# Performance work log

Measured on AMD Instinct MI355X. Metric: run time of the kernel, lower is better.

## Reference

```python
import jax, jax.numpy as jnp
import numpy as np

SM_SCALE = 0.07216878364870322  # 1/sqrt(192)
PAGE_SIZE = 64


def setup_inputs() -> dict:
    key = jax.random.key(0)
    ks = jax.random.split(key, 6)
    B, Hq, Hkv = 32, 16, 1
    DN, DR, DV = 128, 64, 128
    NUM_PAGES, MAX_PAGES = 2048, 64
    return {
        "q": jax.random.normal(ks[0], (B, Hq, DN + DR), dtype=jnp.float32),
        "k_nope_buffer": jax.random.normal(ks[1], (NUM_PAGES, PAGE_SIZE, Hkv, DN), dtype=jnp.float32),
        "k_rope_buffer": jax.random.normal(ks[2], (NUM_PAGES, PAGE_SIZE, Hkv, DR), dtype=jnp.float32),
        "v_buffer": jax.random.normal(ks[3], (NUM_PAGES, PAGE_SIZE, Hkv, DV), dtype=jnp.float32),
        "seq_lens": jax.random.randint(ks[4], (B,), 1, MAX_PAGES * PAGE_SIZE + 1, dtype=jnp.int32),
        "block_table": jax.random.randint(ks[5], (B, MAX_PAGES), 0, NUM_PAGES, dtype=jnp.int32),
    }


def reference(q, k_nope_buffer, k_rope_buffer, v_buffer, seq_lens, block_table):
    B, Hq, _ = q.shape
    Hkv = k_nope_buffer.shape[2]
    dn = k_nope_buffer.shape[-1]
    dv = v_buffer.shape[-1]
    max_kv = block_table.shape[1] * PAGE_SIZE

    q_nope = q[:, :, :dn]            # (B, Hq, dn)
    q_rope = q[:, :, dn:]            # (B, Hq, dr)

    # Gather pages per batch: (B, max_pages, page, Hkv, d) -> (B, max_kv, Hkv, d)
    kn = k_nope_buffer[block_table].reshape(B, max_kv, Hkv, dn)
    kr = k_rope_buffer[block_table].reshape(B, max_kv, Hkv, -1)
    v = v_buffer[block_table].reshape(B, max_kv, Hkv, dv)

    rep = Hq // Hkv  # GQA repeat_interleave == repeat along head axis
    if rep != 1:
        kn = jnp.repeat(kn, rep, axis=2)
        kr = jnp.repeat(kr, rep, axis=2)
        v = jnp.repeat(v, rep, axis=2)

    scores = (jnp.einsum('bhd,bkhd->bhk', q_nope, kn)
              + jnp.einsum('bhd,bkhd->bhk', q_rope, kr)).astype(jnp.float32) * SM_SCALE
    # Mask out key positions beyond each sequence length (replaces per-batch slicing)
    valid = jnp.arange(max_kv)[None, None, :] < seq_lens[:, None, None]
    scores = jnp.where(valid, scores, -jnp.inf)
    probs = jax.nn.softmax(scores, axis=-1).astype(v.dtype)  # (B, Hq, max_kv)
    out = jnp.einsum('bhk,bkhd->bhd', probs, v)              # (B, Hq, dv)
    return out
```

## Files before the change

### kernel.cpp

```cpp
#include <hip/hip_runtime.h>
#include <math.h>

#define NB 32
#define HQ 16
#define DN 128
#define DR 64
#define DQT 192
#define DV 128
#define PAGE 64
#define MAXP 64
#define NSPLIT 16
#define SPLIT_PAGES 4
#define SPLIT_T (SPLIT_PAGES * PAGE)
#define SM_SCALE 0.07216878364870322f

__global__ __launch_bounds__(256, 2)
void attn_partial_kernel(const float* __restrict__ q,
                         const float* __restrict__ kn,
                         const float* __restrict__ kr,
                         const float* __restrict__ v,
                         const int* __restrict__ seq_lens,
                         const int* __restrict__ block_table,
                         float* __restrict__ o_part,
                         float* __restrict__ ml_part)
{
    const int split = blockIdx.x;
    const int b = blockIdx.y;
    const int seq = seq_lens[b];
    const int t0 = split * SPLIT_T;
    if (t0 >= seq) return;

    const int tid = (int)threadIdx.x;
    const int wave = tid >> 6;
    const int lane = tid & 63;

    __shared__ float q_s[HQ * DQT];
    __shared__ float p_s[SPLIT_T][HQ];
    __shared__ float redmax_s[SPLIT_PAGES][HQ];
    __shared__ float redsum_s[SPLIT_PAGES][HQ];
    __shared__ float acc_s[DV][HQ + 1];
    __shared__ int bt_s[SPLIT_PAGES];

    {
        const float4* qb = (const float4*)(q + (size_t)b * HQ * DQT);
        float4* qs4 = (float4*)q_s;
        #pragma unroll
        for (int i = 0; i < 3; i++) qs4[tid + 256 * i] = qb[tid + 256 * i];
    }
    if (tid < SPLIT_PAGES)
        bt_s[tid] = block_table[b * MAXP + split * SPLIT_PAGES + tid];
    __syncthreads();

    float s[HQ];
    #pragma unroll
    for (int h = 0; h < HQ; h++) s[h] = 0.f;

    const int pbase = t0 + wave * PAGE;
    const bool wave_valid = pbase < seq;
    const bool valid = (pbase + lane) < seq;

    if (wave_valid) {
        const int pid = bt_s[wave];
        const float4* knp = (const float4*)(kn + ((size_t)pid * PAGE + lane) * DN);
        #pragma unroll 8
        for (int c = 0; c < DN / 4; c++) {
            float4 k4 = knp[c];
            #pragma unroll
            for (int h = 0; h < HQ; h++) {
                float4 q4 = ((const float4*)(q_s + h * DQT))[c];
                s[h] += q4.x * k4.x + q4.y * k4.y + q4.z * k4.z + q4.w * k4.w;
            }
        }
        const float4* krp = (const float4*)(kr + ((size_t)pid * PAGE + lane) * DR);
        #pragma unroll 8
        for (int c = 0; c < DR / 4; c++) {
            float4 k4 = krp[c];
            #pragma unroll
            for (int h = 0; h < HQ; h++) {
                float4 q4 = ((const float4*)(q_s + h * DQT))[DN / 4 + c];
                s[h] += q4.x * k4.x + q4.y * k4.y + q4.z * k4.z + q4.w * k4.w;
            }
        }
    }
    #pragma unroll
    for (int h = 0; h < HQ; h++) s[h] = valid ? s[h] * SM_SCALE : -INFINITY;

    #pragma unroll
    for (int h = 0; h < HQ; h++) {
        float m = s[h];
        #pragma unroll
        for (int off = 32; off > 0; off >>= 1) m = fmaxf(m, __shfl_xor(m, off));
        if (lane == 0) redmax_s[wave][h] = m;
    }
    __syncthreads();

    #pragma unroll
    for (int h = 0; h < HQ; h++) {
        float m = fmaxf(fmaxf(redmax_s[0][h], redmax_s[1][h]),
                        fmaxf(redmax_s[2][h], redmax_s[3][h]));
        s[h] = __expf(s[h] - m);
    }
    {
        const int t = wave * PAGE + lane;
        float4* prow = (float4*)(&p_s[t][0]);
        #pragma unroll
        for (int j = 0; j < 4; j++) {
            float4 pv;
            pv.x = s[4 * j + 0]; pv.y = s[4 * j + 1];
            pv.z = s[4 * j + 2]; pv.w = s[4 * j + 3];
            prow[j] = pv;
        }
    }
    #pragma unroll
    for (int h = 0; h < HQ; h++) {
        float l = s[h];
        #pragma unroll
        for (int off = 32; off > 0; off >>= 1) l += __shfl_xor(l, off);
        if (lane == 0) redsum_s[wave][h] = l;
    }
    __syncthreads();

    if (tid < HQ) {
        const int h = tid;
        float m = fmaxf(fmaxf(redmax_s[0][h], redmax_s[1][h]),
                        fmaxf(redmax_s[2][h], redmax_s[3][h]));
        float l = redsum_s[0][h] + redsum_s[1][h] + redsum_s[2][h] + redsum_s[3][h];
        float* ml = ml_part + ((size_t)(b * NSPLIT + split) * HQ + h) * 2;
        ml[0] = m;
        ml[1] = l;
    }

    const int g = tid >> 7;
    const int d = tid & 127;
    float acc[HQ];
    #pragma unroll
    for (int h = 0; h < HQ; h++) acc[h] = 0.f;

    #pragma unroll
    for (int w = 0; w < SPLIT_PAGES; w++) {
        const int base = w * PAGE;
        if (t0 + base >= seq) break;
        const int pid = bt_s[w];
        int rem = seq - t0 - base;
        const int lim = rem < PAGE ? rem : PAGE;
        const float* vp = v + (size_t)pid * PAGE * DV + d;
        #pragma unroll 4
        for (int l2 = g; l2 < lim; l2 += 2) {
            float vv = vp[(size_t)l2 * DV];
            const float4* prow = (const float4*)(&p_s[base + l2][0]);
            #pragma unroll
            for (int j = 0; j < 4; j++) {
                float4 p4 = prow[j];
                acc[4 * j + 0] += p4.x * vv;
                acc[4 * j + 1] += p4.y * vv;
                acc[4 * j + 2] += p4.z * vv;
                acc[4 * j + 3] += p4.w * vv;
            }
        }
    }

    if (g == 1) {
        #pragma unroll
        for (int h = 0; h < HQ; h++) acc_s[d][h] = acc[h];
    }
    __syncthreads();
    if (g == 0) {
        float* op = o_part + ((size_t)(b * NSPLIT + split) * HQ) * DV + d;
        #pragma unroll
        for (int h = 0; h < HQ; h++)
            op[h * DV] = acc[h] + acc_s[d][h];
    }
}

__global__ __launch_bounds__(128)
void attn_combine_kernel(const float* __restrict__ o_part,
                         const float* __restrict__ ml_part,
                         const int* __restrict__ seq_lens,
                         float* __restrict__ out)
{
    const int h = blockIdx.x;
    const int b = blockIdx.y;
    const int d = (int)threadIdx.x;
    const int seq = seq_lens[b];
    int ns = (seq + SPLIT_T - 1) / SPLIT_T;
    if (ns > NSPLIT) ns = NSPLIT;

    float M = -INFINITY, den = 0.f, acc = 0.f;
    for (int s2 = 0; s2 < ns; s2++) {
        const float* ml = ml_part + ((size_t)(b * NSPLIT + s2) * HQ + h) * 2;
        float m = ml[0], l = ml[1];
        float o = o_part[((size_t)(b * NSPLIT + s2) * HQ + h) * DV + d];
        float nM = fmaxf(M, m);
        float eo = __expf(M - nM);
        float en = __expf(m - nM);
        acc = acc * eo + o * en;
        den = den * eo + l * en;
        M = nM;
    }
    out[((size_t)b * HQ + h) * DV + d] = acc / den;
}

extern "C" void kernel_launch(void* const* d_in, const int* in_sizes, int n_in,
                              void* d_out, int out_size, void* d_ws, size_t ws_size,
                              hipStream_t stream)
{
    const float* q  = (const float*)d_in[0];
    const float* kn = (const float*)d_in[1];
    const float* kr = (const float*)d_in[2];
    const float* v  = (const float*)d_in[3];
    const int* seq_lens    = (const int*)d_in[4];
    const int* block_table = (const int*)d_in[5];

    float* o_part  = (float*)d_ws;
    float* ml_part = o_part + (size_t)NB * NSPLIT * HQ * DV;

    attn_partial_kernel<<<dim3(NSPLIT, NB), 256, 0, stream>>>(
        q, kn, kr, v, seq_lens, block_table, o_part, ml_part);
    attn_combine_kernel<<<dim3(HQ, NB), 128, 0, stream>>>(
        o_part, ml_part, seq_lens, (float*)d_out);
}
```

Before: 205.9 us.

## Split attention into per-wave page work items with transposed Q in global memory

```diff
diff --git a/kernel.cpp b/kernel.cpp
--- a/kernel.cpp
+++ b/kernel.cpp
@@ -9,13 +9,26 @@
 #define DV 128
 #define PAGE 64
 #define MAXP 64
-#define NSPLIT 16
-#define SPLIT_PAGES 4
-#define SPLIT_T (SPLIT_PAGES * PAGE)
 #define SM_SCALE 0.07216878364870322f
 
+#define WAVE_LDS_FENCE() asm volatile("s_waitcnt lgkmcnt(0)" ::: "memory")
+
+__global__ __launch_bounds__(256)
+void q_transpose_kernel(const float* __restrict__ q, float* __restrict__ qT)
+{
+    int idx = blockIdx.x * 256 + threadIdx.x;
+    if (idx >= NB * 48 * HQ) return;
+    int h = idx & 15;
+    int t = idx >> 4;
+    int c4 = t % 48;
+    int b = t / 48;
+    const float4* q4 = (const float4*)q;
+    ((float4*)qT)[idx] = q4[((size_t)b * HQ + h) * 48 + c4];
+}
+
+template<int PP>
 __global__ __launch_bounds__(256, 2)
-void attn_partial_kernel(const float* __restrict__ q,
+void attn_partial_kernel(const float* __restrict__ qT,
                          const float* __restrict__ kn,
                          const float* __restrict__ kr,
                          const float* __restrict__ v,
@@ -24,50 +37,53 @@
                          float* __restrict__ o_part,
                          float* __restrict__ ml_part)
 {
-    const int split = blockIdx.x;
-    const int b = blockIdx.y;
-    const int seq = seq_lens[b];
-    const int t0 = split * SPLIT_T;
-    if (t0 >= seq) return;
-
+    constexpr int NS = MAXP / PP;
     const int tid = (int)threadIdx.x;
     const int wave = tid >> 6;
     const int lane = tid & 63;
 
-    __shared__ float q_s[HQ * DQT];
-    __shared__ float p_s[SPLIT_T][HQ];
-    __shared__ float redmax_s[SPLIT_PAGES][HQ];
-    __shared__ float redsum_s[SPLIT_PAGES][HQ];
-    __shared__ float acc_s[DV][HQ + 1];
-    __shared__ int bt_s[SPLIT_PAGES];
-
-    {
-        const float4* qb = (const float4*)(q + (size_t)b * HQ * DQT);
-        float4* qs4 = (float4*)q_s;
-        #pragma unroll
-        for (int i = 0; i < 3; i++) qs4[tid + 256 * i] = qb[tid + 256 * i];
-    }
-    if (tid < SPLIT_PAGES)
-        bt_s[tid] = block_table[b * MAXP + split * SPLIT_PAGES + tid];
-    __syncthreads();
-
-    float s[HQ];
+    const int item = blockIdx.x * 4 + wave;
+    const int b = item / NS;
+    const int chunk = item % NS;
+    const int page0 = chunk * PP;
+
+    const int seq = seq_lens[b];
+    if (page0 * PAGE >= seq) return;
+
+    __shared__ float p_s[4][PAGE][HQ];
+
+    const float4* qTb = (const float4*)qT + (size_t)b * 48 * HQ;
+
+    float m_run[HQ], l_run[HQ];
+    float4 accv[HQ];
     #pragma unroll
-    for (int h = 0; h < HQ; h++) s[h] = 0.f;
-
-    const int pbase = t0 + wave * PAGE;
-    const bool wave_valid = pbase < seq;
-    const bool valid = (pbase + lane) < seq;
-
-    if (wave_valid) {
-        const int pid = bt_s[wave];
+    for (int h = 0; h < HQ; h++) {
+        m_run[h] = -INFINITY; l_run[h] = 0.f;
+        accv[h] = make_float4(0.f, 0.f, 0.f, 0.f);
+    }
+
+    const int tg = lane >> 5;
+    const int dq = (lane & 31) * 4;
+
+    #pragma unroll
+    for (int pg = 0; pg < PP; pg++) {
+        const int page = page0 + pg;
+        if (page * PAGE >= seq) break;
+        const int pid = block_table[b * MAXP + page];
+        const bool valid = page * PAGE + lane < seq;
+
+        float s[HQ];
+        #pragma unroll
+        for (int h = 0; h < HQ; h++) s[h] = 0.f;
+
         const float4* knp = (const float4*)(kn + ((size_t)pid * PAGE + lane) * DN);
         #pragma unroll 8
         for (int c = 0; c < DN / 4; c++) {
             float4 k4 = knp[c];
+            const float4* qc = qTb + c * HQ;
             #pragma unroll
             for (int h = 0; h < HQ; h++) {
-                float4 q4 = ((const float4*)(q_s + h * DQT))[c];
+                float4 q4 = qc[h];
                 s[h] += q4.x * k4.x + q4.y * k4.y + q4.z * k4.z + q4.w * k4.w;
             }
         }
@@ -75,126 +91,117 @@
         #pragma unroll 8
         for (int c = 0; c < DR / 4; c++) {
             float4 k4 = krp[c];
+            const float4* qc = qTb + (DN / 4 + c) * HQ;
             #pragma unroll
             for (int h = 0; h < HQ; h++) {
-                float4 q4 = ((const float4*)(q_s + h * DQT))[DN / 4 + c];
+                float4 q4 = qc[h];
                 s[h] += q4.x * k4.x + q4.y * k4.y + q4.z * k4.z + q4.w * k4.w;
             }
         }
-    }
-    #pragma unroll
-    for (int h = 0; h < HQ; h++) s[h] = valid ? s[h] * SM_SCALE : -INFINITY;
+        #pragma unroll
+        for (int h = 0; h < HQ; h++) s[h] = valid ? s[h] * SM_SCALE : -INFINITY;
+
+        float alpha[HQ];
+        #pragma unroll
+        for (int h = 0; h < HQ; h++) {
+            float m = s[h];
+            #pragma unroll
+            for (int off = 32; off > 0; off >>= 1) m = fmaxf(m, __shfl_xor(m, off));
+            float m_new = fmaxf(m_run[h], m);
+            alpha[h] = __expf(m_run[h] - m_new);
+            m_run[h] = m_new;
+            s[h] = __expf(s[h] - m_new);
+            float l = s[h];
+            #pragma unroll
+            for (int off = 32; off > 0; off >>= 1) l += __shfl_xor(l, off);
+            l_run[h] = l_run[h] * alpha[h] + l;
+        }
+
+        WAVE_LDS_FENCE();
+        {
+            float4* prow = (float4*)(&p_s[wave][lane][0]);
+            #pragma unroll
+            for (int j = 0; j < 4; j++)
+                prow[j] = make_float4(s[4*j+0], s[4*j+1], s[4*j+2], s[4*j+3]);
+        }
+        WAVE_LDS_FENCE();
+
+        #pragma unroll
+        for (int h = 0; h < HQ; h++) {
+            accv[h].x *= alpha[h]; accv[h].y *= alpha[h];
+            accv[h].z *= alpha[h]; accv[h].w *= alpha[h];
+        }
+        const float* vp = v + (size_t)pid * PAGE * DV + dq;
+        #pragma unroll 4
+        for (int t = tg; t < PAGE; t += 2) {
+            float4 v4 = *(const float4*)(vp + (size_t)t * DV);
+            const float4* prow = (const float4*)(&p_s[wave][t][0]);
+            #pragma unroll
+            for (int j = 0; j < 4; j++) {
+                float4 p4 = prow[j];
+                accv[4*j+0].x += p4.x * v4.x; accv[4*j+0].y += p4.x * v4.y;
+                accv[4*j+0].z += p4.x * v4.z; accv[4*j+0].w += p4.x * v4.w;
+                accv[4*j+1].x += p4.y * v4.x; accv[4*j+1].y += p4.y * v4.y;
+                accv[4*j+1].z += p4.y * v4.z; accv[4*j+1].w += p4.y * v4.w;
+                accv[4*j+2].x += p4.z * v4.x; accv[4*j+2].y += p4.z * v4.y;
+                accv[4*j+2].z += p4.z * v4.z; accv[4*j+2].w += p4.z * v4.w;
+                accv[4*j+3].x += p4.w * v4.x; accv[4*j+3].y += p4.w * v4.y;
+                accv[4*j+3].z += p4.w * v4.z; accv[4*j+3].w += p4.w * v4.w;
+            }
+        }
+    }
 
     #pragma unroll
     for (int h = 0; h < HQ; h++) {
-        float m = s[h];
-        #pragma unroll
-        for (int off = 32; off > 0; off >>= 1) m = fmaxf(m, __shfl_xor(m, off));
-        if (lane == 0) redmax_s[wave][h] = m;
-    }
-    __syncthreads();
-
-    #pragma unroll
-    for (int h = 0; h < HQ; h++) {
-        float m = fmaxf(fmaxf(redmax_s[0][h], redmax_s[1][h]),
-                        fmaxf(redmax_s[2][h], redmax_s[3][h]));
-        s[h] = __expf(s[h] - m);
-    }
-    {
-        const int t = wave * PAGE + lane;
-        float4* prow = (float4*)(&p_s[t][0]);
-        #pragma unroll
-        for (int j = 0; j < 4; j++) {
-            float4 pv;
-            pv.x = s[4 * j + 0]; pv.y = s[4 * j + 1];
-            pv.z = s[4 * j + 2]; pv.w = s[4 * j + 3];
-            prow[j] = pv;
-        }
-    }
-    #pragma unroll
-    for (int h = 0; h < HQ; h++) {
-        float l = s[h];
-        #pragma unroll
-        for (int off = 32; off > 0; off >>= 1) l += __shfl_xor(l, off);
-        if (lane == 0) redsum_s[wave][h] = l;
-    }
-    __syncthreads();
-
-    if (tid < HQ) {
-        const int h = tid;
-        float m = fmaxf(fmaxf(redmax_s[0][h], redmax_s[1][h]),
-                        fmaxf(redmax_s[2][h], redmax_s[3][h]));
-        float l = redsum_s[0][h] + redsum_s[1][h] + redsum_s[2][h] + redsum_s[3][h];
-        float* ml = ml_part + ((size_t)(b * NSPLIT + split) * HQ + h) * 2;
-        ml[0] = m;
-        ml[1] = l;
-    }
-
-    const int g = tid >> 7;
-    const int d = tid & 127;
-    float acc[HQ];
-    #pragma unroll
-    for (int h = 0; h < HQ; h++) acc[h] = 0.f;
-
-    #pragma unroll
-    for (int w = 0; w < SPLIT_PAGES; w++) {
-        const int base = w * PAGE;
-        if (t0 + base >= seq) break;
-        const int pid = bt_s[w];
-        int rem = seq - t0 - base;
-        const int lim = rem < PAGE ? rem : PAGE;
-        const float* vp = v + (size_t)pid * PAGE * DV + d;
-        #pragma unroll 4
-        for (int l2 = g; l2 < lim; l2 += 2) {
-            float vv = vp[(size_t)l2 * DV];
-            const float4* prow = (const float4*)(&p_s[base + l2][0]);
-            #pragma unroll
-            for (int j = 0; j < 4; j++) {
-                float4 p4 = prow[j];
-                acc[4 * j + 0] += p4.x * vv;
-                acc[4 * j + 1] += p4.y * vv;
-                acc[4 * j + 2] += p4.z * vv;
-                acc[4 * j + 3] += p4.w * vv;
-            }
-        }
-    }
-
-    if (g == 1) {
-        #pragma unroll
-        for (int h = 0; h < HQ; h++) acc_s[d][h] = acc[h];
-    }
-    __syncthreads();
-    if (g == 0) {
-        float* op = o_part + ((size_t)(b * NSPLIT + split) * HQ) * DV + d;
+        accv[h].x += __shfl_xor(accv[h].x, 32);
+        accv[h].y += __shfl_xor(accv[h].y, 32);
+        accv[h].z += __shfl_xor(accv[h].z, 32);
+        accv[h].w += __shfl_xor(accv[h].w, 32);
+    }
+
+    if (lane < 32) {
+        float* op = o_part + ((size_t)(b * NS + chunk) * HQ) * DV + dq;
         #pragma unroll
         for (int h = 0; h < HQ; h++)
-            op[h * DV] = acc[h] + acc_s[d][h];
-    }
-}
-
+            *(float4*)(op + h * DV) = accv[h];
+    }
+    if (lane == 0) {
+        float* ml = ml_part + ((size_t)(b * NS + chunk) * HQ) * 2;
+        #pragma unroll
+        for (int h = 0; h < HQ; h++) {
+            ml[2*h]   = m_run[h];
+            ml[2*h+1] = l_run[h];
+        }
+    }
+}
+
+template<int PP>
 __global__ __launch_bounds__(128)
 void attn_combine_kernel(const float* __restrict__ o_part,
                          const float* __restrict__ ml_part,
                          const int* __restrict__ seq_lens,
                          float* __restrict__ out)
 {
+    constexpr int NS = MAXP / PP;
+    constexpr int SPLIT_T = PP * PAGE;
     const int h = blockIdx.x;
     const int b = blockIdx.y;
     const int d = (int)threadIdx.x;
     const int seq = seq_lens[b];
     int ns = (seq + SPLIT_T - 1) / SPLIT_T;
-    if (ns > NSPLIT) ns = NSPLIT;
+    if (ns > NS) ns = NS;
 
     float M = -INFINITY, den = 0.f, acc = 0.f;
+    #pragma unroll 4
     for (int s2 = 0; s2 < ns; s2++) {
-        const float* ml = ml_part + ((size_t)(b * NSPLIT + s2) * HQ + h) * 2;
-        float m = ml[0], l = ml[1];
-        float o = o_part[((size_t)(b * NSPLIT + s2) * HQ + h) * DV + d];
-        float nM = fmaxf(M, m);
+        const float2 ml = *(const float2*)(ml_part +
+                            ((size_t)(b * NS + s2) * HQ + h) * 2);
+        float o = o_part[((size_t)(b * NS + s2) * HQ + h) * DV + d];
+        float nM = fmaxf(M, ml.x);
         float eo = __expf(M - nM);
-        float en = __expf(m - nM);
+        float en = __expf(ml.x - nM);
         acc = acc * eo + o * en;
-        den = den * eo + l * en;
+        den = den * eo + ml.y * en;
         M = nM;
     }
     out[((size_t)b * HQ + h) * DV + d] = acc / den;
@@ -211,11 +218,29 @@
     const int* seq_lens    = (const int*)d_in[4];
     const int* block_table = (const int*)d_in[5];
 
-    float* o_part  = (float*)d_ws;
-    float* ml_part = o_part + (size_t)NB * NSPLIT * HQ * DV;
-
-    attn_partial_kernel<<<dim3(NSPLIT, NB), 256, 0, stream>>>(
-        q, kn, kr, v, seq_lens, block_table, o_part, ml_part);
-    attn_combine_kernel<<<dim3(HQ, NB), 128, 0, stream>>>(
-        o_part, ml_part, seq_lens, (float*)d_out);
-}
+    const size_t big_need = (size_t)NB * 64 * HQ * DV * 4
+                          + (size_t)NB * 64 * HQ * 2 * 4
+                          + (size_t)NB * 48 * HQ * 4 * 4;
+
+    if (ws_size >= big_need) {
+        constexpr int PP = 1, NS = MAXP / PP;
+        float* o_part  = (float*)d_ws;
+        float* ml_part = o_part + (size_t)NB * NS * HQ * DV;
+        float* qT      = ml_part + (size_t)NB * NS * HQ * 2;
+        q_transpose_kernel<<<(NB*48*HQ + 255)/256, 256, 0, stream>>>(q, qT);
+        attn_partial_kernel<PP><<<NB * NS / 4, 256, 0, stream>>>(
+            qT, kn, kr, v, seq_lens, block_table, o_part, ml_part);
+        attn_combine_kernel<PP><<<dim3(HQ, NB), 128, 0, stream>>>(
+            o_part, ml_part, seq_lens, (float*)d_out);
+    } else {
+        constexpr int PP = 4, NS = MAXP / PP;
+        float* o_part  = (float*)d_ws;
+        float* ml_part = o_part + (size_t)NB * NS * HQ * DV;
+        float* qT      = ml_part + (size_t)NB * NS * HQ * 2;
+        q_transpose_kernel<<<(NB*48*HQ + 255)/256, 256, 0, stream>>>(q, qT);
+        attn_partial_kernel<PP><<<NB * NS / 4, 256, 0, stream>>>(
+            qT, kn, kr, v, seq_lens, block_table, o_part, ml_part);
+        attn_combine_kernel<PP><<<dim3(HQ, NB), 128, 0, stream>>>(
+            o_part, ml_part, seq_lens, (float*)d_out);
+    }
+}
```

Result: slower. 239.8 us (+16.5%).
